# Kernel optimization log

Measured on AMD Instinct MI355X. Metric: run time of the kernel, lower is better.

## Reference

```python
import jax, jax.numpy as jnp
import numpy as np

B, T, C = 2, 2048, 2048
N_HEAD, N_KV = 16, 2
D_HEAD = C // N_HEAD          # 128
R = N_HEAD // N_KV            # q heads per kv head = 8


def setup_inputs() -> dict:
    key = jax.random.key(0)
    ks = jax.random.split(key, 5)
    s = 0.02
    return {
        "x": jax.random.normal(ks[0], (B, T, C), dtype=jnp.float32),
        "Wq": jax.random.normal(ks[1], (C, C), dtype=jnp.float32) * s,
        "Wk": jax.random.normal(ks[2], (C, N_KV * D_HEAD), dtype=jnp.float32) * s,
        "Wv": jax.random.normal(ks[3], (C, N_KV * D_HEAD), dtype=jnp.float32) * s,
        "Wo": jax.random.normal(ks[4], (C, C), dtype=jnp.float32) * s,
    }


def reference(x, Wq, Wk, Wv, Wo):
    b, t, c = x.shape
    # projections (no bias per config.bias=False)
    q = (x @ Wq).reshape(b, t, N_KV, R, D_HEAD)        # group q heads by kv group
    k = (x @ Wk).reshape(b, t, N_KV, D_HEAD)
    v = (x @ Wv).reshape(b, t, N_KV, D_HEAD)
    scale = 1.0 / jnp.sqrt(jnp.float32(D_HEAD))
    # scores: [b, g(kv), r, tq, tk] -- broadcast kv heads instead of repeat_interleave
    att = jnp.einsum('btgrd,bsgd->bgrts', q, k) * scale
    causal = jnp.tril(jnp.ones((t, t), dtype=bool))
    att = jnp.where(causal, att, -jnp.inf)
    att = jax.nn.softmax(att, axis=-1)
    y = jnp.einsum('bgrts,bsgd->btgrd', att, v).reshape(b, t, c)
    return y @ Wo
```

## Files before the change

kernel.cpp:

```cpp
#include <hip/hip_runtime.h>
#include <stdint.h>

using bf16x8 = __attribute__((ext_vector_type(8))) __bf16;
using f32x4  = __attribute__((ext_vector_type(4))) float;
using u32x4  = __attribute__((ext_vector_type(4))) unsigned;

#define GLL(g, l) __builtin_amdgcn_global_load_lds(                                  \
    (const __attribute__((address_space(1))) void*)(g),                              \
    (__attribute__((address_space(3))) void*)(l), 16, 0, 0)

__device__ __forceinline__ unsigned short f2bf(float f) {
  unsigned u = __builtin_bit_cast(unsigned, f);
  u += 0x7FFF + ((u >> 16) & 1);
  return (unsigned short)(u >> 16);
}
__device__ __forceinline__ float bf2f(unsigned short u) {
  unsigned v = ((unsigned)u) << 16;
  return __builtin_bit_cast(float, v);
}

__global__ __launch_bounds__(256) void cast_kernel(const float* __restrict__ in,
                                                   unsigned short* __restrict__ out, int n4) {
  int i = blockIdx.x * 256 + threadIdx.x;
  if (i >= n4) return;
  float4 v = reinterpret_cast<const float4*>(in)[i];
  ushort4 o;
  o.x = f2bf(v.x); o.y = f2bf(v.y); o.z = f2bf(v.z); o.w = f2bf(v.w);
  reinterpret_cast<ushort4*>(out)[i] = o;
}

__global__ __launch_bounds__(256) void tcast_kernel(const float* __restrict__ W,
                                                    unsigned short* __restrict__ Wt,
                                                    int K, int N) {
  __shared__ float T[64][65];
  const int k0 = blockIdx.x * 64, n0 = blockIdx.y * 64;
  const int t = threadIdx.x;
  const int r4 = t >> 6, c = t & 63;
#pragma unroll
  for (int p = 0; p < 16; ++p) {
    int r = p * 4 + r4;
    T[r][c] = W[(size_t)(k0 + r) * N + n0 + c];
  }
  __syncthreads();
#pragma unroll
  for (int p = 0; p < 16; ++p) {
    int r = p * 4 + r4;
    Wt[(size_t)(n0 + r) * K + k0 + c] = f2bf(T[c][r]);
  }
}

__global__ __launch_bounds__(256) void tv_kernel(const unsigned short* __restrict__ V,
                                                 unsigned short* __restrict__ Vt) {
  __shared__ unsigned short T[64][68];
  const int t0 = blockIdx.x * 64;
  const int d0 = blockIdx.y * 64;
  const int t = threadIdx.x;
  const int r4 = t >> 6, c = t & 63;
#pragma unroll
  for (int p = 0; p < 16; ++p) {
    int r = p * 4 + r4;
    T[r][c] = V[(size_t)(t0 + r) * 2560 + 2304 + d0 + c];
  }
  __syncthreads();
  const int b = t0 >> 11;
  const int tl = t0 & 2047;
#pragma unroll
  for (int p = 0; p < 16; ++p) {
    int dr = p * 4 + r4;
    int dg = d0 + dr;
    int g = dg >> 7, dl = dg & 127;
    Vt[(size_t)((b * 2 + g) * 128 + dl) * 2048 + tl + c] = T[c][dr];
  }
}

template <bool FP32OUT>
__global__ __launch_bounds__(256) void gemm_bt_kernel(const unsigned short* __restrict__ A,
                                                      const unsigned short* __restrict__ Bt,
                                                      void* __restrict__ Cout,
                                                      int K, int lda, int ldb, int ldc,
                                                      float scale, int nscale) {
  __shared__ __align__(16) unsigned short As[128 * 64];
  __shared__ __align__(16) unsigned short Bs[128 * 64];
  const int m0 = blockIdx.x * 128, n0 = blockIdx.y * 128;
  const int t = threadIdx.x;
  const int w = t >> 6, lane = t & 63;
  const int l15 = lane & 15, quad = lane >> 4;
  const int wm = (w >> 1) * 64, wn = (w & 1) * 64;

  const int srow = lane >> 3;
  const int sgl = (lane & 7) ^ srow;

  f32x4 acc[4][4] = {};

  for (int k0 = 0; k0 < K; k0 += 64) {
    __syncthreads();
#pragma unroll
    for (int p = 0; p < 4; ++p) {
      int rowbase = p * 32 + w * 8;
      GLL(&A[(size_t)(m0 + rowbase + srow) * lda + k0 + sgl * 8], &As[rowbase * 64]);
      GLL(&Bt[(size_t)(n0 + rowbase + srow) * ldb + k0 + sgl * 8], &Bs[rowbase * 64]);
    }
    __syncthreads();
#pragma unroll
    for (int kk = 0; kk < 64; kk += 32) {
      const int kg = kk >> 3;
      const int phys = ((kg + quad) ^ (l15 & 7)) * 8;
      bf16x8 af[4], bfr[4];
#pragma unroll
      for (int mt = 0; mt < 4; ++mt)
        af[mt] = *reinterpret_cast<const bf16x8*>(&As[(wm + mt * 16 + l15) * 64 + phys]);
#pragma unroll
      for (int nt = 0; nt < 4; ++nt)
        bfr[nt] = *reinterpret_cast<const bf16x8*>(&Bs[(wn + nt * 16 + l15) * 64 + phys]);
#pragma unroll
      for (int mt = 0; mt < 4; ++mt)
#pragma unroll
        for (int nt = 0; nt < 4; ++nt)
          acc[mt][nt] = __builtin_amdgcn_mfma_f32_16x16x32_bf16(af[mt], bfr[nt], acc[mt][nt], 0, 0, 0);
    }
  }

  const float sc = (n0 < nscale) ? scale : 1.0f;
#pragma unroll
  for (int mt = 0; mt < 4; ++mt) {
#pragma unroll
    for (int reg = 0; reg < 4; ++reg) {
      int row = m0 + wm + mt * 16 + quad * 4 + reg;
#pragma unroll
      for (int nt = 0; nt < 4; ++nt) {
        int col = n0 + wn + nt * 16 + l15;
        float v = acc[mt][nt][reg] * sc;
        if (FP32OUT)
          reinterpret_cast<float*>(Cout)[(size_t)row * ldc + col] = v;
        else
          reinterpret_cast<unsigned short*>(Cout)[(size_t)row * ldc + col] = f2bf(v);
      }
    }
  }
}

#define LDQK 2560
__global__ __launch_bounds__(256, 2) void attn_kernel(const unsigned short* __restrict__ Q,
                                                      const unsigned short* __restrict__ Kg,
                                                      const unsigned short* __restrict__ Vt,
                                                      float* __restrict__ O0,
                                                      unsigned short* __restrict__ O1,
                                                      float* __restrict__ L) {
  __shared__ __align__(16) unsigned short Ks[2][64 * 128];
  __shared__ __align__(16) unsigned short Vs[2][128 * 64];

  const int s  = blockIdx.x;
  const int bx = blockIdx.y;
  const int hh = blockIdx.z & 15;
  const int b  = blockIdx.z >> 4;
  const int g  = hh >> 3;
  const int t  = threadIdx.x;
  const int wg = t >> 6, lane = t & 63;
  const int l15 = lane & 15, quad = lane >> 4;

  const unsigned short* Kbase = Kg + (size_t)b * 2048 * LDQK + g * 128;
  const unsigned short* Vbase = Vt + (size_t)(b * 2 + g) * 128 * 2048;

  const int k_r = lane >> 4;
  const int v_r = lane >> 3;

  auto issueK = [&](int tile, unsigned short* dst) {
    const unsigned short* kb = Kbase + (size_t)(tile * 64) * LDQK;
#pragma unroll
    for (int p = 0; p < 4; ++p) {
      int rowbase = p * 16 + wg * 4;
      int row = rowbase + k_r;
      int gl = (lane & 15) ^ (row & 15);
      GLL(&kb[(size_t)row * LDQK + gl * 8], &dst[rowbase * 128]);
    }
  };
  auto issueV = [&](int tile, unsigned short* dst) {
    const unsigned short* vb = Vbase + tile * 64;
#pragma unroll
    for (int p = 0; p < 4; ++p) {
      int rowbase = p * 32 + wg * 8;
      int row = rowbase + v_r;
      int gl = (lane & 7) ^ (row & 7);
      GLL(&vb[(size_t)row * 2048 + gl * 8], &dst[rowbase * 64]);
    }
  };

  int pb = 0;
  issueK(s, Ks[0]);
  issueV(s, Vs[0]);

  for (int ph = 0; ph < 2; ++ph) {
    const int iq = ph ? (15 - bx) : bx;

    bf16x8 qf[2][4];
#pragma unroll
    for (int mi = 0; mi < 2; ++mi) {
      int qrow = iq * 128 + wg * 32 + mi * 16 + l15;
      const unsigned short* qp = &Q[(size_t)(b * 2048 + qrow) * LDQK + hh * 128 + quad * 8];
#pragma unroll
      for (int dk = 0; dk < 4; ++dk)
        qf[mi][dk] = *reinterpret_cast<const bf16x8*>(qp + dk * 32);
    }

    f32x4 o[2][8] = {};
    float l_run[2] = {};

    for (int j = 0; j <= iq; ++j) {
      const int tile = 2 * j + s;
      __syncthreads();
      const int cur = pb, nxt = pb ^ 1;

      if (j < iq) {
        issueK(tile + 2, Ks[nxt]);
        issueV(tile + 2, Vs[nxt]);
      } else if (ph == 0) {
        issueK(s, Ks[nxt]);
        issueV(s, Vs[nxt]);
      }

      f32x4 sc[2][4] = {};
#pragma unroll
      for (int nt = 0; nt < 4; ++nt) {
#pragma unroll
        for (int dk = 0; dk < 4; ++dk) {
          int phys = (dk * 4 + quad) ^ l15;
          bf16x8 kf = *reinterpret_cast<const bf16x8*>(&Ks[cur][(nt * 16 + l15) * 128 + phys * 8]);
          sc[0][nt] = __builtin_amdgcn_mfma_f32_16x16x32_bf16(kf, qf[0][dk], sc[0][nt], 0, 0, 0);
          sc[1][nt] = __builtin_amdgcn_mfma_f32_16x16x32_bf16(kf, qf[1][dk], sc[1][nt], 0, 0, 0);
        }
      }
      if (j == iq) {
#pragma unroll
        for (int mi = 0; mi < 2; ++mi)
#pragma unroll
          for (int nt = 0; nt < 4; ++nt) {
#pragma unroll
            for (int reg = 0; reg < 4; ++reg) {
              int kcol = tile * 64 + nt * 16 + quad * 4 + reg;
              int qr = iq * 128 + wg * 32 + mi * 16 + l15;
              if (kcol > qr) sc[mi][nt][reg] = -1e30f;
            }
          }
      }

#pragma unroll
      for (int kk = 0; kk < 2; ++kk) {
        bf16x8 pf[2];
#pragma unroll
        for (int mi = 0; mi < 2; ++mi) {
          float pe[4], po[4];
#pragma unroll
          for (int reg = 0; reg < 4; ++reg) {
            pe[reg] = __builtin_exp2f(__builtin_fmaf(sc[mi][kk * 2 + 0][reg], 1.44269504f, -23.08312064f));
            po[reg] = __builtin_exp2f(__builtin_fmaf(sc[mi][kk * 2 + 1][reg], 1.44269504f, -23.08312064f));
            l_run[mi] += pe[reg] + po[reg];
          }
          unsigned a0, a1, b0, b1;
          asm("v_cvt_pk_bf16_f32 %0, %1, %2" : "=v"(a0) : "v"(pe[0]), "v"(pe[1]));
          asm("v_cvt_pk_bf16_f32 %0, %1, %2" : "=v"(a1) : "v"(pe[2]), "v"(pe[3]));
          asm("v_cvt_pk_bf16_f32 %0, %1, %2" : "=v"(b0) : "v"(po[0]), "v"(po[1]));
          asm("v_cvt_pk_bf16_f32 %0, %1, %2" : "=v"(b1) : "v"(po[2]), "v"(po[3]));
          asm("v_permlane32_swap_b32 %0, %1" : "+v"(a0), "+v"(b0));
          asm("v_permlane16_swap_b32 %0, %1" : "+v"(a0), "+v"(b0));
          asm("v_permlane32_swap_b32 %0, %1" : "+v"(a1), "+v"(b1));
          asm("v_permlane16_swap_b32 %0, %1" : "+v"(a1), "+v"(b1));
          u32x4 w;
          w[0] = a0;
          w[1] = a1;
          w[2] = b0;
          w[3] = b1;
          pf[mi] = __builtin_bit_cast(bf16x8, w);
        }
#pragma unroll
        for (int dt = 0; dt < 8; ++dt) {
          int phys = ((kk * 4 + quad) ^ (l15 & 7));
          bf16x8 vf = *reinterpret_cast<const bf16x8*>(&Vs[cur][(dt * 16 + l15) * 64 + phys * 8]);
#pragma unroll
          for (int mi = 0; mi < 2; ++mi)
            o[mi][dt] = __builtin_amdgcn_mfma_f32_16x16x32_bf16(pf[mi], vf, o[mi][dt], 0, 0, 0);
        }
      }
      pb ^= 1;
    }

#pragma unroll
    for (int mi = 0; mi < 2; ++mi) {
      l_run[mi] += __shfl_xor(l_run[mi], 16);
      l_run[mi] += __shfl_xor(l_run[mi], 32);
    }

#pragma unroll
    for (int mi = 0; mi < 2; ++mi) {
      if (quad == 0) {
        int lrow = wg * 32 + mi * 16 + l15;
        L[(size_t)s * 65536 + (size_t)(b * 2048 + iq * 128 + lrow) * 16 + hh] = l_run[mi];
      }
#pragma unroll
      for (int reg = 0; reg < 4; ++reg) {
        int row = wg * 32 + mi * 16 + quad * 4 + reg;
        size_t base = (size_t)(b * 2048 + iq * 128 + row) * 2048 + hh * 128;
        if (s == 0) {
#pragma unroll
          for (int dt = 0; dt < 8; ++dt)
            O0[base + dt * 16 + l15] = o[mi][dt][reg];
        } else {
#pragma unroll
          for (int dt = 0; dt < 8; ++dt)
            O1[base + dt * 16 + l15] = f2bf(o[mi][dt][reg]);
        }
      }
    }
  }
}

__global__ __launch_bounds__(256) void merge_kernel(const float* __restrict__ O0,
                                                    unsigned short* __restrict__ O1,
                                                    const float* __restrict__ L) {
  int i4 = blockIdx.x * 256 + threadIdx.x;
  int e = i4 << 2;
  int tr = e >> 11;
  int hh = (e >> 7) & 15;
  float l = L[tr * 16 + hh] + L[65536 + tr * 16 + hh];
  float inv = 1.0f / l;
  float4 a = reinterpret_cast<const float4*>(O0)[i4];
  ushort4 u = reinterpret_cast<const ushort4*>(O1)[i4];
  ushort4 r;
  r.x = f2bf((a.x + bf2f(u.x)) * inv);
  r.y = f2bf((a.y + bf2f(u.y)) * inv);
  r.z = f2bf((a.z + bf2f(u.z)) * inv);
  r.w = f2bf((a.w + bf2f(u.w)) * inv);
  reinterpret_cast<ushort4*>(O1)[i4] = r;
}

extern "C" void kernel_launch(void* const* d_in, const int* in_sizes, int n_in,
                              void* d_out, int out_size, void* d_ws, size_t ws_size,
                              hipStream_t stream) {
  const float* x  = (const float*)d_in[0];
  const float* Wq = (const float*)d_in[1];
  const float* Wk = (const float*)d_in[2];
  const float* Wv = (const float*)d_in[3];
  const float* Wo = (const float*)d_in[4];

  char* ws = (char*)d_ws;
  unsigned short* xb    = (unsigned short*)(ws + 0);
  unsigned short* Wqkvt = (unsigned short*)(ws + 16777216);
  unsigned short* Wot   = (unsigned short*)(ws + 27262976);
  unsigned short* QKVb  = (unsigned short*)(ws + 35651584);
  unsigned short* Vtb   = (unsigned short*)(ws + 56623104);
  float*          Lb    = (float*)(ws + 58720256);
  unsigned short* Yb    = xb;

  cast_kernel<<<8192, 256, 0, stream>>>(x, xb, 2097152);
  tcast_kernel<<<dim3(32, 32), 256, 0, stream>>>(Wq, Wqkvt, 2048, 2048);
  tcast_kernel<<<dim3(32, 4),  256, 0, stream>>>(Wk, Wqkvt + (size_t)2048 * 2048, 2048, 256);
  tcast_kernel<<<dim3(32, 4),  256, 0, stream>>>(Wv, Wqkvt + (size_t)2304 * 2048, 2048, 256);
  tcast_kernel<<<dim3(32, 32), 256, 0, stream>>>(Wo, Wot, 2048, 2048);

  const float qscale = 0.08838834764831845f;
  gemm_bt_kernel<false><<<dim3(32, 20), 256, 0, stream>>>(xb, Wqkvt, QKVb,
                                                          2048, 2048, 2048, 2560, qscale, 2048);
  tv_kernel<<<dim3(64, 4), 256, 0, stream>>>(QKVb, Vtb);
  attn_kernel<<<dim3(2, 8, 32), 256, 0, stream>>>(QKVb, QKVb + 2048, Vtb,
                                                  (float*)d_out, Yb, Lb);
  merge_kernel<<<8192, 256, 0, stream>>>((const float*)d_out, Yb, Lb);
  gemm_bt_kernel<true><<<dim3(32, 16), 256, 0, stream>>>(Yb, Wot, d_out,
                                                         2048, 2048, 2048, 2048, 1.0f, 0);
}
```

Measured before the change: 282.3 us.

## Software-pipeline QK of next tile with softmax-PV of current tile

Restructures the attention inner loop so that the QK^T scores for tile j+1 are computed while the softmax/PV of tile j runs, with K prefetched two tiles ahead and V one ahead using separate buffer rotation. It also adds s_setprio around MFMA bursts to favour matrix issue across waves. The aim is to hide exp/convert latency and LDS waits behind MFMA work, at the cost of more live registers (two score arrays) and more intricate buffer indexing across the two causal phases.

```diff
diff --git a/kernel.cpp b/kernel.cpp
--- a/kernel.cpp
+++ b/kernel.cpp
@@ -185,12 +185,9 @@
     }
   };
 
-  int pb = 0;
-  issueK(s, Ks[0]);
-  issueV(s, Vs[0]);
-
   for (int ph = 0; ph < 2; ++ph) {
     const int iq = ph ? (15 - bx) : bx;
+    const int vb = ph ? ((bx + 1) & 1) : 0;
 
     bf16x8 qf[2][4];
 #pragma unroll
@@ -202,47 +199,49 @@
         qf[mi][dk] = *reinterpret_cast<const bf16x8*>(qp + dk * 32);
     }
 
+    if (ph == 0) {
+      issueK(s, Ks[0]);
+      if (iq >= 1) issueK(s + 2, Ks[1]);
+      issueV(s, Vs[0]);
+    }
+
     f32x4 o[2][8] = {};
     float l_run[2] = {};
-
-    for (int j = 0; j <= iq; ++j) {
-      const int tile = 2 * j + s;
-      __syncthreads();
-      const int cur = pb, nxt = pb ^ 1;
-
-      if (j < iq) {
-        issueK(tile + 2, Ks[nxt]);
-        issueV(tile + 2, Vs[nxt]);
-      } else if (ph == 0) {
-        issueK(s, Ks[nxt]);
-        issueV(s, Vs[nxt]);
-      }
-
-      f32x4 sc[2][4] = {};
+    f32x4 scA[2][4], scB[2][4];
+
+    auto do_qk = [&](f32x4 (&sc)[2][4], const unsigned short* Kbuf, int masktile) {
+#pragma unroll
+      for (int mi = 0; mi < 2; ++mi)
+#pragma unroll
+        for (int nt = 0; nt < 4; ++nt)
+          sc[mi][nt] = f32x4{0.0f, 0.0f, 0.0f, 0.0f};
+      __builtin_amdgcn_s_setprio(1);
 #pragma unroll
       for (int nt = 0; nt < 4; ++nt) {
 #pragma unroll
         for (int dk = 0; dk < 4; ++dk) {
           int phys = (dk * 4 + quad) ^ l15;
-          bf16x8 kf = *reinterpret_cast<const bf16x8*>(&Ks[cur][(nt * 16 + l15) * 128 + phys * 8]);
+          bf16x8 kf = *reinterpret_cast<const bf16x8*>(&Kbuf[(nt * 16 + l15) * 128 + phys * 8]);
           sc[0][nt] = __builtin_amdgcn_mfma_f32_16x16x32_bf16(kf, qf[0][dk], sc[0][nt], 0, 0, 0);
           sc[1][nt] = __builtin_amdgcn_mfma_f32_16x16x32_bf16(kf, qf[1][dk], sc[1][nt], 0, 0, 0);
         }
       }
-      if (j == iq) {
+      __builtin_amdgcn_s_setprio(0);
+      if (masktile >= 0) {
 #pragma unroll
         for (int mi = 0; mi < 2; ++mi)
 #pragma unroll
-          for (int nt = 0; nt < 4; ++nt) {
+          for (int nt = 0; nt < 4; ++nt)
 #pragma unroll
             for (int reg = 0; reg < 4; ++reg) {
-              int kcol = tile * 64 + nt * 16 + quad * 4 + reg;
+              int kcol = masktile * 64 + nt * 16 + quad * 4 + reg;
               int qr = iq * 128 + wg * 32 + mi * 16 + l15;
               if (kcol > qr) sc[mi][nt][reg] = -1e30f;
             }
-          }
-      }
-
+      }
+    };
+
+    auto do_spv = [&](f32x4 (&sc)[2][4], const unsigned short* Vbuf) {
 #pragma unroll
       for (int kk = 0; kk < 2; ++kk) {
         bf16x8 pf[2];
@@ -271,16 +270,44 @@
           w[3] = b1;
           pf[mi] = __builtin_bit_cast(bf16x8, w);
         }
+        __builtin_amdgcn_s_setprio(1);
 #pragma unroll
         for (int dt = 0; dt < 8; ++dt) {
           int phys = ((kk * 4 + quad) ^ (l15 & 7));
-          bf16x8 vf = *reinterpret_cast<const bf16x8*>(&Vs[cur][(dt * 16 + l15) * 64 + phys * 8]);
-#pragma unroll
-          for (int mi = 0; mi < 2; ++mi)
-            o[mi][dt] = __builtin_amdgcn_mfma_f32_16x16x32_bf16(pf[mi], vf, o[mi][dt], 0, 0, 0);
+          bf16x8 vf = *reinterpret_cast<const bf16x8*>(&Vbuf[(dt * 16 + l15) * 64 + phys * 8]);
+          o[0][dt] = __builtin_amdgcn_mfma_f32_16x16x32_bf16(pf[0], vf, o[0][dt], 0, 0, 0);
+          o[1][dt] = __builtin_amdgcn_mfma_f32_16x16x32_bf16(pf[1], vf, o[1][dt], 0, 0, 0);
         }
-      }
-      pb ^= 1;
+        __builtin_amdgcn_s_setprio(0);
+      }
+    };
+
+    __syncthreads();
+    do_qk(scA, Ks[0], (iq == 0) ? s : -1);
+    __syncthreads();
+
+    int j = 0;
+    auto slot = [&](f32x4 (&cur)[2][4], f32x4 (&nxt)[2][4]) {
+      const int tile = 2 * j + s;
+      if (j + 2 <= iq) issueK(tile + 4, Ks[j & 1]);
+      if (j + 1 <= iq) issueV(tile + 2, Vs[((j + 1) & 1) ^ vb]);
+      if (ph == 0 && j == iq) {
+        issueK(s, Ks[0]);
+        issueK(s + 2, Ks[1]);
+        issueV(s, Vs[(bx + 1) & 1]);
+      }
+      if (j < iq)
+        do_qk(nxt, Ks[(j + 1) & 1], (j + 1 == iq) ? (tile + 2) : -1);
+      do_spv(cur, Vs[(j & 1) ^ vb]);
+      __syncthreads();
+    };
+    while (true) {
+      slot(scA, scB);
+      if (j == iq) break;
+      ++j;
+      slot(scB, scA);
+      if (j == iq) break;
+      ++j;
     }
 
 #pragma unroll
```

After: 302.1 us. 1.07x slower.

## Fuse cast and weight-transpose kernels into one prep launch; add MFMA setprio

Applied to the files above, without the earlier changes.

Merges the x cast kernel and the four weight transpose-cast kernels into a single prep_kernel that dispatches on block index, so four launches and their inter-kernel gaps disappear and the small Wk/Wv transposes can overlap with the other work. Separately, the attention kernel raises wave priority with s_setprio around the QK^T and PV MFMA loops so matrix work is scheduled ahead of softmax and load waves. The fused kernel carries a shared-memory array even for the cast blocks, which may lower occupancy for those blocks. The setprio effect depends on how waves interleave.

```diff
diff --git a/kernel.cpp b/kernel.cpp
--- a/kernel.cpp
+++ b/kernel.cpp
@@ -19,22 +19,11 @@
   return __builtin_bit_cast(float, v);
 }
 
-__global__ __launch_bounds__(256) void cast_kernel(const float* __restrict__ in,
-                                                   unsigned short* __restrict__ out, int n4) {
-  int i = blockIdx.x * 256 + threadIdx.x;
-  if (i >= n4) return;
-  float4 v = reinterpret_cast<const float4*>(in)[i];
-  ushort4 o;
-  o.x = f2bf(v.x); o.y = f2bf(v.y); o.z = f2bf(v.z); o.w = f2bf(v.w);
-  reinterpret_cast<ushort4*>(out)[i] = o;
-}
-
-__global__ __launch_bounds__(256) void tcast_kernel(const float* __restrict__ W,
-                                                    unsigned short* __restrict__ Wt,
-                                                    int K, int N) {
-  __shared__ float T[64][65];
-  const int k0 = blockIdx.x * 64, n0 = blockIdx.y * 64;
-  const int t = threadIdx.x;
+__device__ __forceinline__ void tcast_block(const float* __restrict__ W,
+                                            unsigned short* __restrict__ Wt,
+                                            int K, int N, int kb, int nb,
+                                            float (*T)[65], int t) {
+  const int k0 = kb * 64, n0 = nb * 64;
   const int r4 = t >> 6, c = t & 63;
 #pragma unroll
   for (int p = 0; p < 16; ++p) {
@@ -47,6 +36,35 @@
     int r = p * 4 + r4;
     Wt[(size_t)(n0 + r) * K + k0 + c] = f2bf(T[c][r]);
   }
+}
+
+__global__ __launch_bounds__(256) void prep_kernel(const float* __restrict__ x,
+                                                   const float* __restrict__ Wq,
+                                                   const float* __restrict__ Wk,
+                                                   const float* __restrict__ Wv,
+                                                   const float* __restrict__ Wo,
+                                                   unsigned short* __restrict__ xb,
+                                                   unsigned short* __restrict__ Wqkvt,
+                                                   unsigned short* __restrict__ Wot) {
+  __shared__ float T[64][65];
+  int bid = blockIdx.x;
+  const int t = threadIdx.x;
+  if (bid < 8192) {
+    int i = bid * 256 + t;
+    float4 v = reinterpret_cast<const float4*>(x)[i];
+    ushort4 o;
+    o.x = f2bf(v.x); o.y = f2bf(v.y); o.z = f2bf(v.z); o.w = f2bf(v.w);
+    reinterpret_cast<ushort4*>(xb)[i] = o;
+    return;
+  }
+  bid -= 8192;
+  if (bid < 1024) { tcast_block(Wq, Wqkvt, 2048, 2048, bid & 31, bid >> 5, T, t); return; }
+  bid -= 1024;
+  if (bid < 128)  { tcast_block(Wk, Wqkvt + (size_t)2048 * 2048, 2048, 256, bid & 31, bid >> 5, T, t); return; }
+  bid -= 128;
+  if (bid < 128)  { tcast_block(Wv, Wqkvt + (size_t)2304 * 2048, 2048, 256, bid & 31, bid >> 5, T, t); return; }
+  bid -= 128;
+  tcast_block(Wo, Wot, 2048, 2048, bid & 31, bid >> 5, T, t);
 }
 
 __global__ __launch_bounds__(256) void tv_kernel(const unsigned short* __restrict__ V,
@@ -219,6 +237,7 @@
       }
 
       f32x4 sc[2][4] = {};
+      __builtin_amdgcn_s_setprio(1);
 #pragma unroll
       for (int nt = 0; nt < 4; ++nt) {
 #pragma unroll
@@ -229,6 +248,7 @@
           sc[1][nt] = __builtin_amdgcn_mfma_f32_16x16x32_bf16(kf, qf[1][dk], sc[1][nt], 0, 0, 0);
         }
       }
+      __builtin_amdgcn_s_setprio(0);
       if (j == iq) {
 #pragma unroll
         for (int mi = 0; mi < 2; ++mi)
@@ -271,14 +291,15 @@
           w[3] = b1;
           pf[mi] = __builtin_bit_cast(bf16x8, w);
         }
+        __builtin_amdgcn_s_setprio(1);
 #pragma unroll
         for (int dt = 0; dt < 8; ++dt) {
           int phys = ((kk * 4 + quad) ^ (l15 & 7));
           bf16x8 vf = *reinterpret_cast<const bf16x8*>(&Vs[cur][(dt * 16 + l15) * 64 + phys * 8]);
-#pragma unroll
-          for (int mi = 0; mi < 2; ++mi)
-            o[mi][dt] = __builtin_amdgcn_mfma_f32_16x16x32_bf16(pf[mi], vf, o[mi][dt], 0, 0, 0);
+          o[0][dt] = __builtin_amdgcn_mfma_f32_16x16x32_bf16(pf[0], vf, o[0][dt], 0, 0, 0);
+          o[1][dt] = __builtin_amdgcn_mfma_f32_16x16x32_bf16(pf[1], vf, o[1][dt], 0, 0, 0);
         }
+        __builtin_amdgcn_s_setprio(0);
       }
       pb ^= 1;
     }
@@ -350,11 +371,7 @@
   float*          Lb    = (float*)(ws + 58720256);
   unsigned short* Yb    = xb;
 
-  cast_kernel<<<8192, 256, 0, stream>>>(x, xb, 2097152);
-  tcast_kernel<<<dim3(32, 32), 256, 0, stream>>>(Wq, Wqkvt, 2048, 2048);
-  tcast_kernel<<<dim3(32, 4),  256, 0, stream>>>(Wk, Wqkvt + (size_t)2048 * 2048, 2048, 256);
-  tcast_kernel<<<dim3(32, 4),  256, 0, stream>>>(Wv, Wqkvt + (size_t)2304 * 2048, 2048, 256);
-  tcast_kernel<<<dim3(32, 32), 256, 0, stream>>>(Wo, Wot, 2048, 2048);
+  prep_kernel<<<10496, 256, 0, stream>>>(x, Wq, Wk, Wv, Wo, xb, Wqkvt, Wot);
 
   const float qscale = 0.08838834764831845f;
   gemm_bt_kernel<false><<<dim3(32, 20), 256, 0, stream>>>(xb, Wqkvt, QKVb,
```

New measurement: 278.7 us. No clear change (-1.3%).
